# Kernel tuning notes

Hardware: AMD Instinct MI355X
Metric: run time of the kernel (lower is better)

The kernel has to match this reference:

```python
import jax, jax.numpy as jnp
import numpy as np

S_CNT, R_CNT, P_CNT = 10000, 10000, 50000
K_S, K_R, K_P = 64, 64, 128
T = 50
N = 1_000_000


def setup_inputs() -> dict:
    key = jax.random.key(0)
    ks, kr, kp, kt, kws, kwr, kwp = jax.random.split(key, 7)
    s = jax.random.randint(ks, (N,), 0, S_CNT)
    r = jax.random.randint(kr, (N,), 0, R_CNT)
    p = jax.random.randint(kp, (N,), 0, P_CNT)
    t = jax.random.randint(kt, (N,), 0, T)
    X = jnp.stack([s, r, p, t], axis=1).astype(jnp.int64)  # n x 4
    # xavier_uniform-like init: bound = sqrt(6/(fan_in+fan_out))
    def xavier(k, shape):
        bound = np.sqrt(6.0 / (shape[0] + shape[1])).astype(np.float32)
        return jax.random.uniform(k, shape, jnp.float32, -bound, bound)
    s_embeds = xavier(kws, (T * S_CNT, K_S))
    r_embeds = xavier(kwr, (T * R_CNT, K_R))
    p_embeds = xavier(kwp, (P_CNT, K_P))
    return {"X": X, "s_embeds": s_embeds, "r_embeds": r_embeds, "p_embeds": p_embeds}


def reference(X, s_embeds, r_embeds, p_embeds):
    s, r, p, t = X[:, 0], X[:, 1], X[:, 2], X[:, 3]
    st = s + t * S_CNT
    rt = r + t * R_CNT
    se = s_embeds[st]            # [n, K_S]
    re = r_embeds[rt]            # [n, K_R]
    pe = p_embeds[p]             # [n, K_S + K_R]
    # dot(concat(se, re), pe) without materializing the concat
    prod = jnp.sum(se * pe[:, :K_S], axis=1) + jnp.sum(re * pe[:, K_S:], axis=1)
    return jax.nn.sigmoid(prod)  # [n]
```

## Files before the change

### kernel.cpp

```cpp
#include <hip/hip_runtime.h>
#include <cstdint>

#define S_CNT 10000
#define R_CNT 10000
#define PG 1024
#define PROWS 49
#define CAP 1216
#define SPLIT 2
#define PACKED_OFF_B 16384
#define WS_NEED ((size_t)PACKED_OFF_B + 16ull * PG * CAP)

__device__ __forceinline__ unsigned bfpack(float a, float b) {
    unsigned ua = __float_as_uint(a), ub = __float_as_uint(b);
    ua = (ua + 0x7FFFu + ((ua >> 16) & 1u)) >> 16;
    ub = (ub + 0x7FFFu + ((ub >> 16) & 1u)) >> 16;
    return ua | (ub << 16);
}
__device__ __forceinline__ float blo(unsigned u) { return __uint_as_float(u << 16); }
__device__ __forceinline__ float bhi(unsigned u) { return __uint_as_float(u & 0xFFFF0000u); }

__global__ __launch_bounds__(256) void zero_kernel(int4* __restrict__ cur4) {
    cur4[threadIdx.x] = make_int4(0, 0, 0, 0);
}

__global__ __launch_bounds__(256) void bin_kernel(
    const int* __restrict__ X, int n, int* __restrict__ cursors,
    int4* __restrict__ packed,
    const float* __restrict__ se, const float* __restrict__ re,
    const float* __restrict__ pe, float* __restrict__ out)
{
    __shared__ int lhist[PG], lbase[PG], lcur[PG];
    const int tid = threadIdx.x;
    const long long base = (long long)blockIdx.x * 1024;

    #pragma unroll
    for (int k = 0; k < PG / 256; ++k) lhist[tid + 256 * k] = 0;
    __syncthreads();

    int4 xs[4];
    int  grp[4];
    #pragma unroll
    for (int it = 0; it < 4; ++it) {
        const long long i = base + it * 256 + tid;
        if (i < n) {
            xs[it] = *reinterpret_cast<const int4*>(X + 4 * i);
            grp[it] = xs[it].z / PROWS;
            atomicAdd(&lhist[grp[it]], 1);
        } else grp[it] = -1;
    }
    __syncthreads();
    #pragma unroll
    for (int k = 0; k < PG / 256; ++k) {
        const int b = tid + 256 * k;
        const int c = lhist[b];
        lbase[b] = c ? atomicAdd(&cursors[b], c) : 0;
        lcur[b] = 0;
    }
    __syncthreads();
    #pragma unroll
    for (int it = 0; it < 4; ++it) {
        const int g = grp[it];
        if (g < 0) continue;
        const long long i = base + it * 256 + tid;
        const int rank = lbase[g] + atomicAdd(&lcur[g], 1);
        if (rank < CAP) {
            packed[(long long)g * CAP + rank] =
                make_int4(xs[it].x | (xs[it].w << 16), xs[it].y, xs[it].z, (int)i);
        } else {
            const long long st = (long long)xs[it].x + (long long)xs[it].w * S_CNT;
            const long long rt = (long long)xs[it].y + (long long)xs[it].w * R_CNT;
            const long long p  = xs[it].z;
            float acc = 0.f;
            for (int k = 0; k < 64; ++k)
                acc += se[st * 64 + k] * pe[p * 128 + k]
                     + re[rt * 64 + k] * pe[p * 128 + 64 + k];
            out[i] = 1.0f / (1.0f + __expf(-acc));
        }
    }
}

__global__ __launch_bounds__(256, 8) void compute_kernel(
    const int* __restrict__ cursors, const int4* __restrict__ packed,
    const float* __restrict__ s_embeds, const float* __restrict__ r_embeds,
    const float* __restrict__ p_embeds, float* __restrict__ out)
{
    __shared__ __align__(16) unsigned plds[PROWS * 64];
    const int g = blockIdx.x / SPLIT;
    const int q = blockIdx.x % SPLIT;
    const int cnt = min(cursors[g], CAP);
    if (cnt == 0) return;

    const int prow0 = g * PROWS;
    const int rows = min(PROWS, 50000 - prow0);
    const int nf4 = rows * 32;
    const float4* src = reinterpret_cast<const float4*>(p_embeds + (long long)prow0 * 128);
    for (int k = threadIdx.x; k < nf4; k += 256) {
        const float4 v = src[k];
        uint2 u;
        u.x = bfpack(v.x, v.y);
        u.y = bfpack(v.z, v.w);
        reinterpret_cast<uint2*>(plds)[k] = u;
    }
    __syncthreads();

    const int lo  = (int)((long long)cnt * q / SPLIT);
    const int end = (int)((long long)cnt * (q + 1) / SPLIT);
    if (lo >= end) return;

    const int gl = threadIdx.x >> 4;
    const int l  = threadIdx.x & 15;
    const int4* pk = packed + (long long)g * CAP;

    for (int sb = lo; sb < end; sb += 32) {
        const int jA = sb + gl;
        const int jB = sb + 16 + gl;
        const int4 a = pk[min(jA, end - 1)];
        const int4 b = pk[min(jB, end - 1)];

        const int sA = a.x & 0xFFFF, tA = a.x >> 16;
        const int sB = b.x & 0xFFFF, tB = b.x >> 16;
        const int stA = sA + tA * S_CNT, rtA = a.y + tA * R_CNT;
        const int stB = sB + tB * S_CNT, rtB = b.y + tB * R_CNT;

        const float4 seA = *reinterpret_cast<const float4*>(s_embeds + (long long)stA * 64 + l * 4);
        const float4 reA = *reinterpret_cast<const float4*>(r_embeds + (long long)rtA * 64 + l * 4);
        const float4 seB = *reinterpret_cast<const float4*>(s_embeds + (long long)stB * 64 + l * 4);
        const float4 reB = *reinterpret_cast<const float4*>(r_embeds + (long long)rtB * 64 + l * 4);

        const int pA32 = (a.z - prow0) * 64;
        const int pB32 = (b.z - prow0) * 64;
        const uint2 uplA = *reinterpret_cast<const uint2*>(&plds[pA32 + l * 2]);
        const uint2 uphA = *reinterpret_cast<const uint2*>(&plds[pA32 + 32 + l * 2]);
        const uint2 uplB = *reinterpret_cast<const uint2*>(&plds[pB32 + l * 2]);
        const uint2 uphB = *reinterpret_cast<const uint2*>(&plds[pB32 + 32 + l * 2]);

        float accA = seA.x * blo(uplA.x) + seA.y * bhi(uplA.x)
                   + seA.z * blo(uplA.y) + seA.w * bhi(uplA.y)
                   + reA.x * blo(uphA.x) + reA.y * bhi(uphA.x)
                   + reA.z * blo(uphA.y) + reA.w * bhi(uphA.y);
        float accB = seB.x * blo(uplB.x) + seB.y * bhi(uplB.x)
                   + seB.z * blo(uplB.y) + seB.w * bhi(uplB.y)
                   + reB.x * blo(uphB.x) + reB.y * bhi(uphB.x)
                   + reB.z * blo(uphB.y) + reB.w * bhi(uphB.y);

        accA += __shfl_xor(accA, 1, 64);  accB += __shfl_xor(accB, 1, 64);
        accA += __shfl_xor(accA, 2, 64);  accB += __shfl_xor(accB, 2, 64);
        accA += __shfl_xor(accA, 4, 64);  accB += __shfl_xor(accB, 4, 64);
        accA += __shfl_xor(accA, 8, 64);  accB += __shfl_xor(accB, 8, 64);

        if (l == 0 && jA < end) out[a.w] = 1.0f / (1.0f + __expf(-accA));
        if (l == 0 && jB < end) out[b.w] = 1.0f / (1.0f + __expf(-accB));
    }
}

__global__ __launch_bounds__(256) void direct_kernel(
    const int* __restrict__ X,
    const float* __restrict__ s_embeds, const float* __restrict__ r_embeds,
    const float* __restrict__ p_embeds, float* __restrict__ out, int n) {
    const int g = threadIdx.x >> 4;
    const int l = threadIdx.x & 15;
    const int i = blockIdx.x * 16 + g;
    if (i >= n) return;
    const int4 xi = *reinterpret_cast<const int4*>(X + 4ll * i);
    const long long st = (long long)xi.x + (long long)xi.w * S_CNT;
    const long long rt = (long long)xi.y + (long long)xi.w * R_CNT;
    const long long p  = xi.z;
    const float4 se = *reinterpret_cast<const float4*>(s_embeds + st * 64 + l * 4);
    const float4 re = *reinterpret_cast<const float4*>(r_embeds + rt * 64 + l * 4);
    const float4 pl = *reinterpret_cast<const float4*>(p_embeds + p * 128 + l * 4);
    const float4 ph = *reinterpret_cast<const float4*>(p_embeds + p * 128 + 64 + l * 4);
    float acc = se.x * pl.x + se.y * pl.y + se.z * pl.z + se.w * pl.w
              + re.x * ph.x + re.y * ph.y + re.z * ph.z + re.w * ph.w;
    acc += __shfl_xor(acc, 1, 64);
    acc += __shfl_xor(acc, 2, 64);
    acc += __shfl_xor(acc, 4, 64);
    acc += __shfl_xor(acc, 8, 64);
    if (l == 0) out[i] = 1.0f / (1.0f + __expf(-acc));
}

extern "C" void kernel_launch(void* const* d_in, const int* in_sizes, int n_in,
                              void* d_out, int out_size, void* d_ws, size_t ws_size,
                              hipStream_t stream) {
    const int*   X        = (const int*)d_in[0];
    const float* s_embeds = (const float*)d_in[1];
    const float* r_embeds = (const float*)d_in[2];
    const float* p_embeds = (const float*)d_in[3];
    float* out = (float*)d_out;
    const int n = in_sizes[0] / 4;

    if (ws_size < WS_NEED) {
        direct_kernel<<<(n + 15) / 16, 256, 0, stream>>>(
            X, s_embeds, r_embeds, p_embeds, out, n);
        return;
    }

    int* cursors = (int*)d_ws;
    int4* packed = reinterpret_cast<int4*>((char*)d_ws + PACKED_OFF_B);

    zero_kernel<<<1, 256, 0, stream>>>(reinterpret_cast<int4*>(cursors));
    bin_kernel<<<(n + 1023) / 1024, 256, 0, stream>>>(
        X, n, cursors, packed, s_embeds, r_embeds, p_embeds, out);
    compute_kernel<<<PG * SPLIT, 256, 0, stream>>>(
        cursors, packed, s_embeds, r_embeds, p_embeds, out);
}
```

Before: 141.6 us.

## Pack binned records into 8 bytes and process four records per thread group

Binned records shrink from a 16-byte int4 to an 8-byte int2 by bit-packing s, t, the local p offset, r and the output index, which halves the scatter writes and the re-reads of the packed buffer. The compute loop now gives each 16-lane group four consecutive records loaded with two vector loads, and issues all eight embedding gathers before any math so more memory requests are in flight. The split point between the two blocks of a bin is aligned to 64. The packing relies on fixed field widths (s and r under 16384, t under 64, n under 2^24), and holding four records per thread raises register pressure.

```diff
diff --git a/kernel.cpp b/kernel.cpp
--- a/kernel.cpp
+++ b/kernel.cpp
@@ -8,7 +8,7 @@
 #define CAP 1216
 #define SPLIT 2
 #define PACKED_OFF_B 16384
-#define WS_NEED ((size_t)PACKED_OFF_B + 16ull * PG * CAP)
+#define WS_NEED ((size_t)PACKED_OFF_B + 8ull * PG * CAP)
 
 __device__ __forceinline__ unsigned bfpack(float a, float b) {
     unsigned ua = __float_as_uint(a), ub = __float_as_uint(b);
@@ -25,7 +25,7 @@
 
 __global__ __launch_bounds__(256) void bin_kernel(
     const int* __restrict__ X, int n, int* __restrict__ cursors,
-    int4* __restrict__ packed,
+    int2* __restrict__ packed,
     const float* __restrict__ se, const float* __restrict__ re,
     const float* __restrict__ pe, float* __restrict__ out)
 {
@@ -61,11 +61,13 @@
     for (int it = 0; it < 4; ++it) {
         const int g = grp[it];
         if (g < 0) continue;
-        const long long i = base + it * 256 + tid;
+        const unsigned i = (unsigned)(base + it * 256 + tid);
         const int rank = lbase[g] + atomicAdd(&lcur[g], 1);
         if (rank < CAP) {
-            packed[(long long)g * CAP + rank] =
-                make_int4(xs[it].x | (xs[it].w << 16), xs[it].y, xs[it].z, (int)i);
+            const unsigned dp = (unsigned)(xs[it].z - g * PROWS);
+            packed[g * CAP + rank] = make_int2(
+                (int)((unsigned)xs[it].x | ((unsigned)xs[it].w << 14) | (dp << 20) | ((i & 63u) << 26)),
+                (int)((unsigned)xs[it].y | ((i >> 6) << 14)));
         } else {
             const long long st = (long long)xs[it].x + (long long)xs[it].w * S_CNT;
             const long long rt = (long long)xs[it].y + (long long)xs[it].w * R_CNT;
@@ -80,7 +82,7 @@
 }
 
 __global__ __launch_bounds__(256, 8) void compute_kernel(
-    const int* __restrict__ cursors, const int4* __restrict__ packed,
+    const int* __restrict__ cursors, const int2* __restrict__ packed,
     const float* __restrict__ s_embeds, const float* __restrict__ r_embeds,
     const float* __restrict__ p_embeds, float* __restrict__ out)
 {
@@ -103,53 +105,74 @@
     }
     __syncthreads();
 
-    const int lo  = (int)((long long)cnt * q / SPLIT);
-    const int end = (int)((long long)cnt * (q + 1) / SPLIT);
+    const int mid = (cnt / 2) & ~63;
+    const int lo  = (q == 0) ? 0 : mid;
+    const int end = (q == 0) ? mid : cnt;
     if (lo >= end) return;
 
     const int gl = threadIdx.x >> 4;
     const int l  = threadIdx.x & 15;
-    const int4* pk = packed + (long long)g * CAP;
-
-    for (int sb = lo; sb < end; sb += 32) {
-        const int jA = sb + gl;
-        const int jB = sb + 16 + gl;
-        const int4 a = pk[min(jA, end - 1)];
-        const int4 b = pk[min(jB, end - 1)];
-
-        const int sA = a.x & 0xFFFF, tA = a.x >> 16;
-        const int sB = b.x & 0xFFFF, tB = b.x >> 16;
-        const int stA = sA + tA * S_CNT, rtA = a.y + tA * R_CNT;
-        const int stB = sB + tB * S_CNT, rtB = b.y + tB * R_CNT;
-
-        const float4 seA = *reinterpret_cast<const float4*>(s_embeds + (long long)stA * 64 + l * 4);
-        const float4 reA = *reinterpret_cast<const float4*>(r_embeds + (long long)rtA * 64 + l * 4);
-        const float4 seB = *reinterpret_cast<const float4*>(s_embeds + (long long)stB * 64 + l * 4);
-        const float4 reB = *reinterpret_cast<const float4*>(r_embeds + (long long)rtB * 64 + l * 4);
-
-        const int pA32 = (a.z - prow0) * 64;
-        const int pB32 = (b.z - prow0) * 64;
-        const uint2 uplA = *reinterpret_cast<const uint2*>(&plds[pA32 + l * 2]);
-        const uint2 uphA = *reinterpret_cast<const uint2*>(&plds[pA32 + 32 + l * 2]);
-        const uint2 uplB = *reinterpret_cast<const uint2*>(&plds[pB32 + l * 2]);
-        const uint2 uphB = *reinterpret_cast<const uint2*>(&plds[pB32 + 32 + l * 2]);
-
-        float accA = seA.x * blo(uplA.x) + seA.y * bhi(uplA.x)
-                   + seA.z * blo(uplA.y) + seA.w * bhi(uplA.y)
-                   + reA.x * blo(uphA.x) + reA.y * bhi(uphA.x)
-                   + reA.z * blo(uphA.y) + reA.w * bhi(uphA.y);
-        float accB = seB.x * blo(uplB.x) + seB.y * bhi(uplB.x)
-                   + seB.z * blo(uplB.y) + seB.w * bhi(uplB.y)
-                   + reB.x * blo(uphB.x) + reB.y * bhi(uphB.x)
-                   + reB.z * blo(uphB.y) + reB.w * bhi(uphB.y);
-
-        accA += __shfl_xor(accA, 1, 64);  accB += __shfl_xor(accB, 1, 64);
-        accA += __shfl_xor(accA, 2, 64);  accB += __shfl_xor(accB, 2, 64);
-        accA += __shfl_xor(accA, 4, 64);  accB += __shfl_xor(accB, 4, 64);
-        accA += __shfl_xor(accA, 8, 64);  accB += __shfl_xor(accB, 8, 64);
-
-        if (l == 0 && jA < end) out[a.w] = 1.0f / (1.0f + __expf(-accA));
-        if (l == 0 && jB < end) out[b.w] = 1.0f / (1.0f + __expf(-accB));
+    const int2* pk = packed + g * CAP;
+
+    for (int sb = lo; sb < end; sb += 64) {
+        const int j0 = sb + gl * 4;
+        int2 rec[4];
+        if (j0 + 3 < end) {
+            const int4 w01 = *reinterpret_cast<const int4*>(pk + j0);
+            const int4 w23 = *reinterpret_cast<const int4*>(pk + j0 + 2);
+            rec[0] = make_int2(w01.x, w01.y); rec[1] = make_int2(w01.z, w01.w);
+            rec[2] = make_int2(w23.x, w23.y); rec[3] = make_int2(w23.z, w23.w);
+        } else {
+            #pragma unroll
+            for (int k = 0; k < 4; ++k) rec[k] = pk[min(j0 + k, end - 1)];
+        }
+
+        int st[4], rt[4], dp[4], idx[4];
+        #pragma unroll
+        for (int k = 0; k < 4; ++k) {
+            const unsigned w0 = (unsigned)rec[k].x, w1 = (unsigned)rec[k].y;
+            const int s = w0 & 0x3FFF;
+            const int t = (w0 >> 14) & 0x3F;
+            dp[k]  = (w0 >> 20) & 0x3F;
+            idx[k] = (int)((w0 >> 26) | ((w1 >> 14) << 6));
+            const int r = w1 & 0x3FFF;
+            st[k] = s + t * S_CNT;
+            rt[k] = r + t * R_CNT;
+        }
+
+        float4 se[4], re[4];
+        #pragma unroll
+        for (int k = 0; k < 4; ++k)
+            se[k] = *reinterpret_cast<const float4*>(s_embeds + (unsigned)st[k] * 64u + l * 4);
+        #pragma unroll
+        for (int k = 0; k < 4; ++k)
+            re[k] = *reinterpret_cast<const float4*>(r_embeds + (unsigned)rt[k] * 64u + l * 4);
+
+        float acc[4];
+        #pragma unroll
+        for (int k = 0; k < 4; ++k) {
+            const int pb = dp[k] * 64;
+            const uint2 upl = *reinterpret_cast<const uint2*>(&plds[pb + l * 2]);
+            const uint2 uph = *reinterpret_cast<const uint2*>(&plds[pb + 32 + l * 2]);
+            acc[k] = se[k].x * blo(upl.x) + se[k].y * bhi(upl.x)
+                   + se[k].z * blo(upl.y) + se[k].w * bhi(upl.y)
+                   + re[k].x * blo(uph.x) + re[k].y * bhi(uph.x)
+                   + re[k].z * blo(uph.y) + re[k].w * bhi(uph.y);
+        }
+
+        #pragma unroll
+        for (int k = 0; k < 4; ++k) {
+            acc[k] += __shfl_xor(acc[k], 1, 64);
+            acc[k] += __shfl_xor(acc[k], 2, 64);
+            acc[k] += __shfl_xor(acc[k], 4, 64);
+            acc[k] += __shfl_xor(acc[k], 8, 64);
+        }
+
+        if (l == 0) {
+            #pragma unroll
+            for (int k = 0; k < 4; ++k)
+                if (j0 + k < end) out[idx[k]] = 1.0f / (1.0f + __expf(-acc[k]));
+        }
     }
 }
 
@@ -195,7 +218,7 @@
     }
 
     int* cursors = (int*)d_ws;
-    int4* packed = reinterpret_cast<int4*>((char*)d_ws + PACKED_OFF_B);
+    int2* packed = reinterpret_cast<int2*>((char*)d_ws + PACKED_OFF_B);
 
     zero_kernel<<<1, 256, 0, stream>>>(reinterpret_cast<int4*>(cursors));
     bin_kernel<<<(n + 1023) / 1024, 256, 0, stream>>>(
```

Measured after the change: 143.4 us. About the same (+1.3%).
